# Kernel optimization log

Measured on AMD Instinct MI355X. Metric: run time of the kernel, lower is better.

## Reference

```python
import jax, jax.numpy as jnp
import numpy as np

B, S, E, H, A = 2, 1024, 1024, 16, 3
HD = E // H

def setup_inputs() -> dict:
    key = jax.random.key(0)
    ks = jax.random.split(key, 8)
    return {
        "query": jax.random.normal(ks[0], (B, S, E), dtype=jnp.float32),
        "key": jax.random.normal(ks[1], (B, S, E), dtype=jnp.float32),
        "value": jax.random.normal(ks[2], (B, S, E), dtype=jnp.float32),
        "aid": jax.random.normal(ks[3], (B, S, S, A), dtype=jnp.float32),
        "mixer_w": jax.random.uniform(ks[4], (H, A + 1, 1), dtype=jnp.float32),
        "mixer_b": jax.random.uniform(ks[5], (H, 1), dtype=jnp.float32),
        "Wo": jax.random.normal(ks[6], (E, E), dtype=jnp.float32) * 0.02,
        "bo": jax.random.normal(ks[7], (E,), dtype=jnp.float32) * 0.02,
        "aid_scale": jnp.array([0.1], dtype=jnp.float32),
    }

def reference(query, key, value, aid, mixer_w, mixer_b, Wo, bo, aid_scale):
    scale = HD ** -0.5
    # Faithful to source: raw row-major reshape (B,S,E)->(B,H,S,HD)
    q = query.reshape(B, H, S, HD)
    k = key.reshape(B, H, S, HD)
    v = value.reshape(B, H, S, HD)
    attn = jnp.einsum('bhqd,bhkd->bhqk', q, k) * scale  # (B,H,S,S)
    aid_h = jnp.broadcast_to(aid[:, None], (B, H, S, S, A))
    mix_in = jnp.concatenate([attn[..., None], aid_h], axis=-1)  # (B,H,S,S,A+1)
    mixed = jnp.einsum('bhqki,hio->bhqko', mix_in, mixer_w) + mixer_b[None, :, None, None, :]
    mixed = jax.nn.relu(mixed)[..., 0]  # (B,H,S,S)
    attn = attn + mixed * aid_scale[0]
    pre_softmax_attn = attn
    attn = jax.nn.softmax(attn, axis=-1)
    out = jnp.einsum('bhqk,bhkd->bhqd', attn, v)
    out = out.transpose(0, 2, 1, 3).reshape(B, S, E)
    out = out @ Wo.T + bo
    return out, attn, pre_softmax_attn
```

## Files before the change

### kernel.cpp

```cpp
#include <hip/hip_runtime.h>
#include <hip/hip_bf16.h>

using u16 = unsigned short;
typedef __attribute__((ext_vector_type(8))) short short8;
typedef __attribute__((ext_vector_type(4))) float f32x4;

constexpr int Bc = 2, Sc = 1024, Ec = 1024, Hc = 16, HDc = 64;
constexpr float SCALE = 0.125f;

__device__ __forceinline__ u16 f2bf(float f) {
    union { float f; unsigned u; } v{f};
    unsigned r = v.u + 0x7FFF + ((v.u >> 16) & 1);
    return (u16)(r >> 16);
}
__device__ __forceinline__ float bf2f(u16 x) {
    union { unsigned u; float f; } v; v.u = ((unsigned)x) << 16; return v.f;
}

__global__ __launch_bounds__(256) void k_prep(
    const float* __restrict__ Q, const float* __restrict__ K,
    const float* __restrict__ Wo, u16* __restrict__ Qb,
    u16* __restrict__ Kb, u16* __restrict__ Wob)
{
    const int bid = blockIdx.x;
    const float* src; u16* dst; int base;
    if (bid < 1024)      { src = Q;  dst = Qb;  base = bid; }
    else if (bid < 2048) { src = K;  dst = Kb;  base = bid - 1024; }
    else                 { src = Wo; dst = Wob; base = bid - 2048; }
    const int i = (base * 256 + threadIdx.x) * 8;
    float4 a = *(const float4*)&src[i];
    float4 b = *(const float4*)&src[i + 4];
    u16 t[8] = {f2bf(a.x), f2bf(a.y), f2bf(a.z), f2bf(a.w),
                f2bf(b.x), f2bf(b.y), f2bf(b.z), f2bf(b.w)};
    *(short8*)&dst[i] = *(short8*)t;
}

__global__ __launch_bounds__(256) void k_convT(const float* __restrict__ V,
                                               u16* __restrict__ Vt) {
    __shared__ float tile[64][65];
    const int bh = blockIdx.y;
    const int k0 = blockIdx.x * 64;
    const float* Vp = V + (size_t)bh * Sc * HDc + (size_t)k0 * HDc;
    const int tid = threadIdx.x;

    #pragma unroll
    for (int it = 0; it < 4; ++it) {
        int idx = tid + it * 256;
        int k = idx >> 4, d4 = idx & 15;
        float4 v = *(const float4*)&Vp[k * HDc + d4 * 4];
        tile[d4 * 4 + 0][k] = v.x;
        tile[d4 * 4 + 1][k] = v.y;
        tile[d4 * 4 + 2][k] = v.z;
        tile[d4 * 4 + 3][k] = v.w;
    }
    __syncthreads();

    u16* Op = Vt + (size_t)bh * HDc * Sc + k0;
    #pragma unroll
    for (int it = 0; it < 4; ++it) {
        int idx = tid + it * 256;
        int d = idx >> 4, kq = idx & 15;
        u16 t[4];
        #pragma unroll
        for (int j = 0; j < 4; ++j) t[j] = f2bf(tile[d][kq * 4 + j]);
        *(uint2*)&Op[(size_t)d * Sc + kq * 4] = *(uint2*)t;
    }
}

__global__ __launch_bounds__(256, 2) void k_scores(
    const u16* __restrict__ Qb, const u16* __restrict__ Kb,
    const float* __restrict__ aid, const float* __restrict__ mw,
    const float* __restrict__ mb, const float* __restrict__ ascale,
    float* __restrict__ pre)
{
    __shared__ u16 Qs[64 * 64];
    __shared__ u16 Ks[64 * 64];

    const int bid = blockIdx.x;
    const int kt = bid & 15;
    const int qt = (bid >> 4) & 15;
    const int b  = bid >> 8;

    const int tid = threadIdx.x;
    const int w = tid >> 6, lane = tid & 63;
    const int lrow = lane & 15, lhi = lane >> 4;

    float a3[4][4][3];
    #pragma unroll
    for (int r = 0; r < 4; ++r) {
        const size_t qg = (size_t)(b * Sc + qt * 64 + w * 16 + lhi * 4 + r) * Sc;
        #pragma unroll
        for (int fk = 0; fk < 4; ++fk) {
            const float* ap = aid + (qg + kt * 64 + fk * 16 + lrow) * 3;
            float2 t2 = *(const float2*)ap;
            a3[r][fk][0] = t2.x; a3[r][fk][1] = t2.y; a3[r][fk][2] = ap[2];
        }
    }

    const float asc = ascale[0];
    const u16* Qbase = Qb + ((size_t)b * Hc * Sc + qt * 64) * HDc;
    const u16* Kbase = Kb + ((size_t)b * Hc * Sc + kt * 64) * HDc;

    for (int h = 0; h < Hc; ++h) {
        const u16* Qp = Qbase + (size_t)h * Sc * HDc;
        const u16* Kp = Kbase + (size_t)h * Sc * HDc;
        #pragma unroll
        for (int it = 0; it < 2; ++it) {
            int idx = tid + it * 256;
            int r = idx >> 3, g = idx & 7;
            int gs = (g ^ (r & 7)) * 8;
            *(short8*)&Qs[r * 64 + gs] = *(const short8*)&Qp[r * 64 + g * 8];
            *(short8*)&Ks[r * 64 + gs] = *(const short8*)&Kp[r * 64 + g * 8];
        }
        __syncthreads();

        f32x4 acc[4] = {};
        #pragma unroll
        for (int ks2 = 0; ks2 < 2; ++ks2) {
            const int rq = w * 16 + lrow;
            short8 af = *(const short8*)&Qs[rq * 64 + ((ks2 * 4 + lhi) ^ (rq & 7)) * 8];
            #pragma unroll
            for (int fk = 0; fk < 4; ++fk) {
                const int rk = fk * 16 + lrow;
                short8 bf = *(const short8*)&Ks[rk * 64 + ((ks2 * 4 + lhi) ^ (rk & 7)) * 8];
                acc[fk] = __builtin_amdgcn_mfma_f32_16x16x32_bf16(af, bf, acc[fk], 0, 0, 0);
            }
        }

        const float w0 = mw[h * 4 + 0], w1 = mw[h * 4 + 1];
        const float w2 = mw[h * 4 + 2], w3 = mw[h * 4 + 3];
        const float bias = mb[h];
        float* prow0 = pre + ((size_t)(b * Hc + h) * Sc + qt * 64 + w * 16 + lhi * 4) * Sc
                     + kt * 64 + lrow;
        #pragma unroll
        for (int r = 0; r < 4; ++r) {
            #pragma unroll
            for (int fk = 0; fk < 4; ++fk) {
                float s = acc[fk][r] * SCALE;
                float mm = s * w0 + a3[r][fk][0] * w1 + a3[r][fk][1] * w2
                         + a3[r][fk][2] * w3 + bias;
                prow0[(size_t)r * Sc + fk * 16] = s + fmaxf(mm, 0.f) * asc;
            }
        }
        __syncthreads();
    }
}

__global__ __launch_bounds__(512, 1) void k_spv(
    const float* __restrict__ pre, const u16* __restrict__ Vt,
    float* __restrict__ attn, u16* __restrict__ Omid)
{
    __shared__ u16 band[64 * 1024];
    __shared__ float s_m[64], s_l[64];

    const int bid = blockIdx.x;
    const int bh  = bid >> 4;
    const int qt  = (bid & 15) * 64;
    const int b   = bh >> 4, h = bh & 15;

    const int tid  = threadIdx.x;
    const int w    = tid >> 6, lane = tid & 63;
    const int lrow = lane & 15, lhi = lane >> 4;

    const int arow_i = tid >> 3;
    const int sub    = tid & 7;
    const int asw    = arow_i & 7;
    const float* prow = pre + ((size_t)bh * Sc + qt + arow_i) * Sc;
    float m = -1e30f;
    #pragma unroll 4
    for (int kt = 0; kt < 16; ++kt) {
        const float* p0 = prow + kt * 64 + sub * 8;
        float s[8];
        *(float4*)&s[0] = *(const float4*)p0;
        *(float4*)&s[4] = *(const float4*)(p0 + 4);
        u16 t[8];
        #pragma unroll
        for (int j = 0; j < 8; ++j) { m = fmaxf(m, s[j]); t[j] = f2bf(s[j]); }
        *(short8*)&band[arow_i * 1024 + (kt * 8 + (sub ^ asw)) * 8] = *(short8*)t;
    }
    m = fmaxf(m, __shfl_xor(m, 1));
    m = fmaxf(m, __shfl_xor(m, 2));
    m = fmaxf(m, __shfl_xor(m, 4));
    if (sub == 0) s_m[arow_i] = m;
    __syncthreads();

    const int rf = w >> 1, dh = w & 1;
    const int brow = rf * 16 + lrow;
    const int bsw  = brow & 7;
    const float mreg = s_m[brow];
    const u16* Vbase = Vt + (size_t)bh * HDc * Sc;
    float l = 0.f;
    f32x4 acc[2] = {};

    #pragma unroll 4
    for (int kt = 0; kt < 16; ++kt) {
        short8 ra = *(const short8*)&band[brow * 1024 + (kt * 8 + (lhi ^ bsw)) * 8];
        short8 rb = *(const short8*)&band[brow * 1024 + (kt * 8 + ((lhi + 4) ^ bsw)) * 8];
        u16 ea[8], eb[8];
        #pragma unroll
        for (int j = 0; j < 8; ++j) {
            float va = __expf(bf2f((u16)ra[j]) - mreg); l += va; ea[j] = f2bf(va);
            float vb = __expf(bf2f((u16)rb[j]) - mreg); l += vb; eb[j] = f2bf(vb);
        }
        short8 A0 = *(short8*)ea, A1 = *(short8*)eb;
        #pragma unroll
        for (int fd = 0; fd < 2; ++fd) {
            const int rv = dh * 32 + fd * 16 + lrow;
            const u16* vp = Vbase + (size_t)rv * Sc + kt * 64;
            short8 b0 = *(const short8*)&vp[lhi * 8];
            short8 b1 = *(const short8*)&vp[(lhi + 4) * 8];
            acc[fd] = __builtin_amdgcn_mfma_f32_16x16x32_bf16(A0, b0, acc[fd], 0, 0, 0);
            acc[fd] = __builtin_amdgcn_mfma_f32_16x16x32_bf16(A1, b1, acc[fd], 0, 0, 0);
        }
    }
    l += __shfl_xor(l, 16);
    l += __shfl_xor(l, 32);
    if (dh == 0 && lhi == 0) s_l[brow] = l;
    __syncthreads();

    const float mf  = s_m[arow_i];
    const float inv = 1.f / s_l[arow_i];
    float* arow = attn + ((size_t)bh * Sc + qt + arow_i) * Sc;
    #pragma unroll 4
    for (int kt = 0; kt < 16; ++kt) {
        short8 ra = *(const short8*)&band[arow_i * 1024 + (kt * 8 + (sub ^ asw)) * 8];
        float o[8];
        #pragma unroll
        for (int j = 0; j < 8; ++j) o[j] = __expf(bf2f((u16)ra[j]) - mf) * inv;
        *(float4*)&arow[kt * 64 + sub * 8]     = *(float4*)&o[0];
        *(float4*)&arow[kt * 64 + sub * 8 + 4] = *(float4*)&o[4];
    }

    #pragma unroll
    for (int reg = 0; reg < 4; ++reg) {
        const int rowO = rf * 16 + lhi * 4 + reg;
        const float linv = 1.f / s_l[rowO];
        u16* orow = Omid + ((size_t)b * Sc + qt + rowO) * Ec + h * HDc + dh * 32;
        #pragma unroll
        for (int fd = 0; fd < 2; ++fd)
            orow[fd * 16 + lrow] = f2bf(acc[fd][reg] * linv);
    }
}

__global__ __launch_bounds__(256, 2) void k_proj(
    const u16* __restrict__ Ob, const u16* __restrict__ Wob,
    const float* __restrict__ bo, float* __restrict__ out)
{
    __shared__ u16 Xs[128 * 64];
    __shared__ u16 Ws[64 * 64];

    const int bid = blockIdx.x;
    const int mt = (bid >> 4) * 128;
    const int et = (bid & 15) * 64;

    const int tid = threadIdx.x;
    const int w = tid >> 6, lane = tid & 63;
    const int lrow = lane & 15, lhi = lane >> 4;

    f32x4 acc[2][4] = {};

    for (int kb = 0; kb < Ec; kb += 64) {
        #pragma unroll
        for (int it = 0; it < 4; ++it) {
            int idx = tid + it * 256;
            int r = idx >> 3, g = idx & 7;
            *(short8*)&Xs[r * 64 + (g ^ (r & 7)) * 8] =
                *(const short8*)&Ob[(size_t)(mt + r) * Ec + kb + g * 8];
        }
        #pragma unroll
        for (int it = 0; it < 2; ++it) {
            int idx = tid + it * 256;
            int r = idx >> 3, g = idx & 7;
            *(short8*)&Ws[r * 64 + (g ^ (r & 7)) * 8] =
                *(const short8*)&Wob[(size_t)(et + r) * Ec + kb + g * 8];
        }
        __syncthreads();

        #pragma unroll
        for (int ks = 0; ks < 2; ++ks) {
            short8 af[2], bfr[4];
            int g = ks * 4 + lhi;
            #pragma unroll
            for (int fq = 0; fq < 2; ++fq) {
                int rq = w * 32 + fq * 16 + lrow;
                af[fq] = *(const short8*)&Xs[rq * 64 + (g ^ (rq & 7)) * 8];
            }
            #pragma unroll
            for (int fd = 0; fd < 4; ++fd) {
                int rv = fd * 16 + lrow;
                bfr[fd] = *(const short8*)&Ws[rv * 64 + (g ^ (rv & 7)) * 8];
            }
            #pragma unroll
            for (int fq = 0; fq < 2; ++fq)
                #pragma unroll
                for (int fd = 0; fd < 4; ++fd)
                    acc[fq][fd] = __builtin_amdgcn_mfma_f32_16x16x32_bf16(
                        af[fq], bfr[fd], acc[fq][fd], 0, 0, 0);
        }
        __syncthreads();
    }

    #pragma unroll
    for (int fq = 0; fq < 2; ++fq)
        #pragma unroll
        for (int r = 0; r < 4; ++r) {
            const int m = mt + w * 32 + fq * 16 + lhi * 4 + r;
            float* orow = out + (size_t)m * Ec + et;
            #pragma unroll
            for (int fd = 0; fd < 4; ++fd) {
                int e = fd * 16 + lrow;
                orow[e] = acc[fq][fd][r] + bo[et + e];
            }
        }
}

extern "C" void kernel_launch(void* const* d_in, const int* in_sizes, int n_in,
                              void* d_out, int out_size, void* d_ws, size_t ws_size,
                              hipStream_t stream) {
    const float* query  = (const float*)d_in[0];
    const float* key    = (const float*)d_in[1];
    const float* value  = (const float*)d_in[2];
    const float* aid    = (const float*)d_in[3];
    const float* mw     = (const float*)d_in[4];
    const float* mb     = (const float*)d_in[5];
    const float* Wo     = (const float*)d_in[6];
    const float* bo     = (const float*)d_in[7];
    const float* ascale = (const float*)d_in[8];

    float* out_p  = (float*)d_out;
    float* attn_p = out_p + (size_t)Bc * Sc * Ec;
    float* pre_p  = attn_p + (size_t)Bc * Hc * Sc * Sc;

    u16* Vtb  = (u16*)d_ws;
    u16* Omid = Vtb  + (size_t)2 * 1024 * 1024;
    u16* Qb   = Omid + (size_t)2 * 1024 * 1024;
    u16* Kb   = Qb   + (size_t)2 * 1024 * 1024;
    u16* Wob  = Kb   + (size_t)2 * 1024 * 1024;

    k_prep<<<2560, 256, 0, stream>>>(query, key, Wo, Qb, Kb, Wob);
    k_convT<<<dim3(Sc / 64, Bc * Hc), 256, 0, stream>>>(value, Vtb);
    k_scores<<<Bc * 16 * 16, 256, 0, stream>>>(Qb, Kb, aid, mw, mb, ascale, pre_p);
    k_spv<<<512, 512, 0, stream>>>(pre_p, Vtb, attn_p, Omid);
    k_proj<<<(Bc * Sc / 128) * (Ec / 64), 256, 0, stream>>>(Omid, Wob, bo, out_p);
}
```

Measured before the change: 147.9 us.

## Halve softmax-PV query tile for occupancy and prefetch next head's Q/K in scores

```diff
diff --git a/kernel.cpp b/kernel.cpp
--- a/kernel.cpp
+++ b/kernel.cpp
@@ -101,18 +101,36 @@
     const u16* Qbase = Qb + ((size_t)b * Hc * Sc + qt * 64) * HDc;
     const u16* Kbase = Kb + ((size_t)b * Hc * Sc + kt * 64) * HDc;
 
+    const int r0 = tid >> 3,          g0 = tid & 7;
+    const int r1 = (tid + 256) >> 3,  g1 = tid & 7;
+    const int gs0 = (g0 ^ (r0 & 7)) * 8;
+    const int gs1 = (g1 ^ (r1 & 7)) * 8;
+
+    short8 qp0, qp1, kp0, kp1;
+    {
+        const u16* Qp = Qbase;
+        const u16* Kp = Kbase;
+        qp0 = *(const short8*)&Qp[r0 * 64 + g0 * 8];
+        qp1 = *(const short8*)&Qp[r1 * 64 + g1 * 8];
+        kp0 = *(const short8*)&Kp[r0 * 64 + g0 * 8];
+        kp1 = *(const short8*)&Kp[r1 * 64 + g1 * 8];
+    }
+
     for (int h = 0; h < Hc; ++h) {
-        const u16* Qp = Qbase + (size_t)h * Sc * HDc;
-        const u16* Kp = Kbase + (size_t)h * Sc * HDc;
-        #pragma unroll
-        for (int it = 0; it < 2; ++it) {
-            int idx = tid + it * 256;
-            int r = idx >> 3, g = idx & 7;
-            int gs = (g ^ (r & 7)) * 8;
-            *(short8*)&Qs[r * 64 + gs] = *(const short8*)&Qp[r * 64 + g * 8];
-            *(short8*)&Ks[r * 64 + gs] = *(const short8*)&Kp[r * 64 + g * 8];
-        }
+        *(short8*)&Qs[r0 * 64 + gs0] = qp0;
+        *(short8*)&Qs[r1 * 64 + gs1] = qp1;
+        *(short8*)&Ks[r0 * 64 + gs0] = kp0;
+        *(short8*)&Ks[r1 * 64 + gs1] = kp1;
         __syncthreads();
+
+        if (h < Hc - 1) {
+            const u16* Qp = Qbase + (size_t)(h + 1) * Sc * HDc;
+            const u16* Kp = Kbase + (size_t)(h + 1) * Sc * HDc;
+            qp0 = *(const short8*)&Qp[r0 * 64 + g0 * 8];
+            qp1 = *(const short8*)&Qp[r1 * 64 + g1 * 8];
+            kp0 = *(const short8*)&Kp[r0 * 64 + g0 * 8];
+            kp1 = *(const short8*)&Kp[r1 * 64 + g1 * 8];
+        }
 
         f32x4 acc[4] = {};
         #pragma unroll
@@ -146,51 +164,55 @@
     }
 }
 
-__global__ __launch_bounds__(512, 1) void k_spv(
+__global__ __launch_bounds__(512, 4) void k_spv(
     const float* __restrict__ pre, const u16* __restrict__ Vt,
     float* __restrict__ attn, u16* __restrict__ Omid)
 {
-    __shared__ u16 band[64 * 1024];
-    __shared__ float s_m[64], s_l[64];
+    __shared__ u16 band[32 * 1024];
+    __shared__ float s_m[32], s_l[32];
 
     const int bid = blockIdx.x;
-    const int bh  = bid >> 4;
-    const int qt  = (bid & 15) * 64;
+    const int bh  = bid >> 5;
+    const int qt  = (bid & 31) * 32;
     const int b   = bh >> 4, h = bh & 15;
 
     const int tid  = threadIdx.x;
     const int w    = tid >> 6, lane = tid & 63;
     const int lrow = lane & 15, lhi = lane >> 4;
 
-    const int arow_i = tid >> 3;
-    const int sub    = tid & 7;
-    const int asw    = arow_i & 7;
-    const float* prow = pre + ((size_t)bh * Sc + qt + arow_i) * Sc;
+    const int arow = tid >> 4;
+    const int s16  = tid & 15;
+    const int g    = s16 & 7;
+    const int kh   = s16 >> 3;
+    const int asw  = arow & 7;
+    const float* prow = pre + ((size_t)bh * Sc + qt + arow) * Sc;
     float m = -1e30f;
-    #pragma unroll 4
-    for (int kt = 0; kt < 16; ++kt) {
-        const float* p0 = prow + kt * 64 + sub * 8;
+    #pragma unroll
+    for (int k2 = 0; k2 < 8; ++k2) {
+        const int kt = kh * 8 + k2;
+        const float* p0 = prow + kt * 64 + g * 8;
         float s[8];
         *(float4*)&s[0] = *(const float4*)p0;
         *(float4*)&s[4] = *(const float4*)(p0 + 4);
         u16 t[8];
         #pragma unroll
         for (int j = 0; j < 8; ++j) { m = fmaxf(m, s[j]); t[j] = f2bf(s[j]); }
-        *(short8*)&band[arow_i * 1024 + (kt * 8 + (sub ^ asw)) * 8] = *(short8*)t;
+        *(short8*)&band[arow * 1024 + (kt * 8 + (g ^ asw)) * 8] = *(short8*)t;
     }
     m = fmaxf(m, __shfl_xor(m, 1));
     m = fmaxf(m, __shfl_xor(m, 2));
     m = fmaxf(m, __shfl_xor(m, 4));
-    if (sub == 0) s_m[arow_i] = m;
+    m = fmaxf(m, __shfl_xor(m, 8));
+    if (s16 == 0) s_m[arow] = m;
     __syncthreads();
 
-    const int rf = w >> 1, dh = w & 1;
+    const int rf = w & 1, df = w >> 1;
     const int brow = rf * 16 + lrow;
     const int bsw  = brow & 7;
     const float mreg = s_m[brow];
-    const u16* Vbase = Vt + (size_t)bh * HDc * Sc;
+    const u16* vrow = Vt + (size_t)bh * HDc * Sc + (size_t)(df * 16 + lrow) * Sc;
     float l = 0.f;
-    f32x4 acc[2] = {};
+    f32x4 acc = {};
 
     #pragma unroll 4
     for (int kt = 0; kt < 16; ++kt) {
@@ -203,42 +225,36 @@
             float vb = __expf(bf2f((u16)rb[j]) - mreg); l += vb; eb[j] = f2bf(vb);
         }
         short8 A0 = *(short8*)ea, A1 = *(short8*)eb;
-        #pragma unroll
-        for (int fd = 0; fd < 2; ++fd) {
-            const int rv = dh * 32 + fd * 16 + lrow;
-            const u16* vp = Vbase + (size_t)rv * Sc + kt * 64;
-            short8 b0 = *(const short8*)&vp[lhi * 8];
-            short8 b1 = *(const short8*)&vp[(lhi + 4) * 8];
-            acc[fd] = __builtin_amdgcn_mfma_f32_16x16x32_bf16(A0, b0, acc[fd], 0, 0, 0);
-            acc[fd] = __builtin_amdgcn_mfma_f32_16x16x32_bf16(A1, b1, acc[fd], 0, 0, 0);
-        }
+        short8 b0 = *(const short8*)&vrow[kt * 64 + lhi * 8];
+        short8 b1 = *(const short8*)&vrow[kt * 64 + (lhi + 4) * 8];
+        acc = __builtin_amdgcn_mfma_f32_16x16x32_bf16(A0, b0, acc, 0, 0, 0);
+        acc = __builtin_amdgcn_mfma_f32_16x16x32_bf16(A1, b1, acc, 0, 0, 0);
     }
     l += __shfl_xor(l, 16);
     l += __shfl_xor(l, 32);
-    if (dh == 0 && lhi == 0) s_l[brow] = l;
+    if (df == 0 && lhi == 0) s_l[brow] = l;
     __syncthreads();
 
-    const float mf  = s_m[arow_i];
-    const float inv = 1.f / s_l[arow_i];
-    float* arow = attn + ((size_t)bh * Sc + qt + arow_i) * Sc;
-    #pragma unroll 4
-    for (int kt = 0; kt < 16; ++kt) {
-        short8 ra = *(const short8*)&band[arow_i * 1024 + (kt * 8 + (sub ^ asw)) * 8];
+    const float mf  = s_m[arow];
+    const float inv = 1.f / s_l[arow];
+    float* arowp = attn + ((size_t)bh * Sc + qt + arow) * Sc;
+    #pragma unroll
+    for (int k2 = 0; k2 < 8; ++k2) {
+        const int kt = kh * 8 + k2;
+        short8 ra = *(const short8*)&band[arow * 1024 + (kt * 8 + (g ^ asw)) * 8];
         float o[8];
         #pragma unroll
         for (int j = 0; j < 8; ++j) o[j] = __expf(bf2f((u16)ra[j]) - mf) * inv;
-        *(float4*)&arow[kt * 64 + sub * 8]     = *(float4*)&o[0];
-        *(float4*)&arow[kt * 64 + sub * 8 + 4] = *(float4*)&o[4];
+        *(float4*)&arowp[kt * 64 + g * 8]     = *(float4*)&o[0];
+        *(float4*)&arowp[kt * 64 + g * 8 + 4] = *(float4*)&o[4];
     }
 
     #pragma unroll
     for (int reg = 0; reg < 4; ++reg) {
         const int rowO = rf * 16 + lhi * 4 + reg;
         const float linv = 1.f / s_l[rowO];
-        u16* orow = Omid + ((size_t)b * Sc + qt + rowO) * Ec + h * HDc + dh * 32;
-        #pragma unroll
-        for (int fd = 0; fd < 2; ++fd)
-            orow[fd * 16 + lrow] = f2bf(acc[fd][reg] * linv);
+        u16* orow = Omid + ((size_t)b * Sc + qt + rowO) * Ec + h * HDc;
+        orow[df * 16 + lrow] = f2bf(acc[reg] * linv);
     }
 }
 
@@ -340,6 +356,6 @@
     k_prep<<<2560, 256, 0, stream>>>(query, key, Wo, Qb, Kb, Wob);
     k_convT<<<dim3(Sc / 64, Bc * Hc), 256, 0, stream>>>(value, Vtb);
     k_scores<<<Bc * 16 * 16, 256, 0, stream>>>(Qb, Kb, aid, mw, mb, ascale, pre_p);
-    k_spv<<<512, 512, 0, stream>>>(pre_p, Vtb, attn_p, Omid);
+    k_spv<<<Bc * Hc * (Sc / 32), 512, 0, stream>>>(pre_p, Vtb, attn_p, Omid);
     k_proj<<<(Bc * Sc / 128) * (Ec / 64), 256, 0, stream>>>(Omid, Wob, bo, out_p);
 }
```

New measurement: 144.2 us. 1.03x faster.
